# Optimization experiments

Hardware: AMD Instinct MI355X
Metric: run time of the kernel (lower is better)

## Reference

```python
import math
import jax, jax.numpy as jnp
import numpy as np

B, S, D, N, H = 4, 1024, 1024, 16, 64

def setup_inputs() -> dict:
    key = jax.random.key(0)
    ks = jax.random.split(key, 10)
    sc = 0.02
    return {
        'from_tensor': jax.random.normal(ks[0], (B, S, D), jnp.float32),
        'to_tensor': jax.random.normal(ks[1], (B, S, D), jnp.float32),
        'attention_mask': jnp.ones((B, S, S), jnp.int32),
        'wq': jax.random.normal(ks[2], (D, N, H), jnp.float32) * sc,
        'bq': jnp.zeros((N, H), jnp.float32),
        'wk': jax.random.normal(ks[3], (D, N, H), jnp.float32) * sc,
        'bk': jnp.zeros((N, H), jnp.float32),
        'wv': jax.random.normal(ks[4], (D, N, H), jnp.float32) * sc,
        'bv': jnp.zeros((N, H), jnp.float32),
        'pre_softmax_weight': jax.random.normal(ks[5], (N, N), jnp.float32) * sc,
        'post_softmax_weight': jax.random.normal(ks[6], (N, N), jnp.float32) * sc,
        'wo': jax.random.normal(ks[7], (N, H, D), jnp.float32) * sc,
        'bo': jnp.zeros((D,), jnp.float32),
    }

def reference(from_tensor, to_tensor, attention_mask, wq, bq, wk, bk, wv, bv,
              pre_softmax_weight, post_softmax_weight, wo, bo):
    # QKV projections: [B,S,D] x [D,N,H] -> [B,S,N,H]
    q = jnp.einsum('bfd,dnh->bfnh', from_tensor, wq) + bq
    k = jnp.einsum('btd,dnh->btnh', to_tensor, wk) + bk
    v = jnp.einsum('btd,dnh->btnh', to_tensor, wv) + bv
    # attention scores [B,N,F,T]
    scores = jnp.einsum('btnh,bfnh->bnft', k, q) * (1.0 / math.sqrt(float(H)))
    # pre-softmax head mixing
    scores = jnp.einsum('bnft,nl->blft', scores, pre_softmax_weight)
    # masked softmax (mask expanded at axis 1, additive -10000 on masked)
    mask = attention_mask.astype(scores.dtype)[:, None, :, :]  # [B,1,F,T]
    scores = scores + (1.0 - mask) * -10000.0
    probs = jax.nn.softmax(scores, axis=-1)
    # post-softmax head mixing (dropout rate 0.0 -> identity)
    probs = jnp.einsum('bnft,nl->blft', probs, post_softmax_weight)
    # attend to values and project out
    ctx = jnp.einsum('bnft,btnh->bfnh', probs, v)
    out = jnp.einsum('bfnh,nhd->bfd', ctx, wo) + bo
    return out
```

## Files before the change

kernel.cpp:

```cpp
#include <hip/hip_runtime.h>
#include <hip/hip_bf16.h>

typedef __hip_bfloat16 bf16;
using short8 = __attribute__((ext_vector_type(8))) short;
using f32x4  = __attribute__((ext_vector_type(4))) float;
using f32x2  = __attribute__((ext_vector_type(2))) float;

#ifndef __has_builtin
#define __has_builtin(x) 0
#endif
#if __has_builtin(__builtin_amdgcn_global_load_lds)
#define HAVE_GLL 1
#else
#define HAVE_GLL 0
#endif

__device__ inline void stage16(const short* __restrict__ g, short* l, int lane) {
#if HAVE_GLL
  __builtin_amdgcn_global_load_lds((__attribute__((address_space(1))) void*)g,
                                   (__attribute__((address_space(3))) void*)l,
                                   16, 0, 0);
#else
  *(short8*)(l + lane * 8) = *(const short8*)g;
#endif
}

__device__ inline unsigned pack2bf(float a, float b) {
  bf16 h0 = __float2bfloat16(a), h1 = __float2bfloat16(b);
  return (unsigned)*(unsigned short*)&h0 | ((unsigned)*(unsigned short*)&h1 << 16);
}

__global__ __launch_bounds__(256) void gemm_lds64(
    const bf16* __restrict__ Ag, long a_bs1, long a_bs2, int lda,
    const bf16* __restrict__ Bg, long b_bs1, long b_bs2, int ldb,
    void* __restrict__ Cg, long c_bs1, long c_bs2, int ldc,
    const float* __restrict__ bias, int K, int Z2, float alpha, int cf32)
{
  __shared__ short As[128 * 64];
  __shared__ short Bs[64 * 64];

  int z = blockIdx.z, z1 = z / Z2, z2 = z - z1 * Z2;
  const short* A = (const short*)(Ag + z1 * a_bs1 + z2 * a_bs2);
  const short* B = (const short*)(Bg + z1 * b_bs1 + z2 * b_bs2);

  int tid = threadIdx.x, lane = tid & 63, w = tid >> 6;
  int wm = w & 1, wn = w >> 1;
  int m0 = blockIdx.x * 128, n0 = blockIdx.y * 64;
  int r = lane & 15, q = lane >> 4;

  int srow = lane >> 3, scol = (lane & 7) * 8;
  const short* Asrc = A + (long)(m0 + w * 32 + srow) * lda + scol;
  const short* Bsrc = B + (long)(n0 + w * 16 + srow) * ldb + scol;
  short* Adst = As + (w * 32) * 64;
  short* Bdst = Bs + (w * 16) * 64;

  f32x4 acc[4][2];
  #pragma unroll
  for (int i = 0; i < 4; ++i)
    #pragma unroll
    for (int j = 0; j < 2; ++j) acc[i][j] = (f32x4){0.f, 0.f, 0.f, 0.f};

  for (int kt = 0; kt < K; kt += 64) {
    #pragma unroll
    for (int i = 0; i < 4; ++i)
      stage16(Asrc + (long)i * 8 * lda + kt, Adst + i * 8 * 64, lane);
    #pragma unroll
    for (int i = 0; i < 2; ++i)
      stage16(Bsrc + (long)i * 8 * ldb + kt, Bdst + i * 8 * 64, lane);
    __syncthreads();
    #pragma unroll
    for (int kk = 0; kk < 64; kk += 32) {
      short8 af[4], bfr[2];
      #pragma unroll
      for (int i = 0; i < 4; ++i)
        af[i] = *(const short8*)&As[(wm * 64 + i * 16 + r) * 64 + kk + q * 8];
      #pragma unroll
      for (int j = 0; j < 2; ++j)
        bfr[j] = *(const short8*)&Bs[(wn * 32 + j * 16 + r) * 64 + kk + q * 8];
      #pragma unroll
      for (int i = 0; i < 4; ++i)
        #pragma unroll
        for (int j = 0; j < 2; ++j)
          acc[i][j] = __builtin_amdgcn_mfma_f32_16x16x32_bf16(af[i], bfr[j], acc[i][j], 0, 0, 0);
    }
    __syncthreads();
  }

  long cb = z1 * c_bs1 + z2 * c_bs2;
  #pragma unroll
  for (int j = 0; j < 2; ++j) {
    int col = n0 + wn * 32 + j * 16 + r;
    float bv = bias ? bias[col] : 0.0f;
    #pragma unroll
    for (int i = 0; i < 4; ++i) {
      int row0 = m0 + wm * 64 + i * 16 + q * 4;
      #pragma unroll
      for (int rr = 0; rr < 4; ++rr) {
        float val = acc[i][j][rr] * alpha + bv;
        long idx = cb + (long)(row0 + rr) * ldc + col;
        if (cf32) ((float*)Cg)[idx] = val;
        else ((bf16*)Cg)[idx] = __float2bfloat16(val);
      }
    }
  }
}

struct QKVArgs {
  const bf16* A[3];
  const bf16* Bw[3];
  bf16* C[3];
  const float* bias[3];
};

__global__ __launch_bounds__(256) void gemm_qkv(QKVArgs args) {
  __shared__ short As[128 * 64];
  __shared__ short Bs[64 * 64];

  int z = blockIdx.z;
  const short* A = (const short*)args.A[z];
  const short* B = (const short*)args.Bw[z];
  bf16* C = args.C[z];
  const float* bias = args.bias[z];

  int tid = threadIdx.x, lane = tid & 63, w = tid >> 6;
  int wm = w & 1, wn = w >> 1;
  int m0 = blockIdx.x * 128, n0 = blockIdx.y * 64;
  int r = lane & 15, q = lane >> 4;

  int srow = lane >> 3, scol = (lane & 7) * 8;
  const short* Asrc = A + (long)(m0 + w * 32 + srow) * 1024 + scol;
  const short* Bsrc = B + (long)(n0 + w * 16 + srow) * 1024 + scol;
  short* Adst = As + (w * 32) * 64;
  short* Bdst = Bs + (w * 16) * 64;

  f32x4 acc[4][2];
  #pragma unroll
  for (int i = 0; i < 4; ++i)
    #pragma unroll
    for (int j = 0; j < 2; ++j) acc[i][j] = (f32x4){0.f, 0.f, 0.f, 0.f};

  for (int kt = 0; kt < 1024; kt += 64) {
    #pragma unroll
    for (int i = 0; i < 4; ++i)
      stage16(Asrc + (long)i * 8 * 1024 + kt, Adst + i * 8 * 64, lane);
    #pragma unroll
    for (int i = 0; i < 2; ++i)
      stage16(Bsrc + (long)i * 8 * 1024 + kt, Bdst + i * 8 * 64, lane);
    __syncthreads();
    #pragma unroll
    for (int kk = 0; kk < 64; kk += 32) {
      short8 af[4], bfr[2];
      #pragma unroll
      for (int i = 0; i < 4; ++i)
        af[i] = *(const short8*)&As[(wm * 64 + i * 16 + r) * 64 + kk + q * 8];
      #pragma unroll
      for (int j = 0; j < 2; ++j)
        bfr[j] = *(const short8*)&Bs[(wn * 32 + j * 16 + r) * 64 + kk + q * 8];
      #pragma unroll
      for (int i = 0; i < 4; ++i)
        #pragma unroll
        for (int j = 0; j < 2; ++j)
          acc[i][j] = __builtin_amdgcn_mfma_f32_16x16x32_bf16(af[i], bfr[j], acc[i][j], 0, 0, 0);
    }
    __syncthreads();
  }

  #pragma unroll
  for (int j = 0; j < 2; ++j) {
    int col = n0 + wn * 32 + j * 16 + r;
    float bv = bias[col];
    #pragma unroll
    for (int i = 0; i < 4; ++i) {
      int row0 = m0 + wm * 64 + i * 16 + q * 4;
      #pragma unroll
      for (int rr = 0; rr < 4; ++rr)
        C[(long)(row0 + rr) * 1024 + col] = __float2bfloat16(acc[i][j][rr] + bv);
    }
  }
}

__global__ __launch_bounds__(256) void gemm_k64(
    const bf16* __restrict__ Ag, long a_bs1, long a_bs2, int lda,
    const bf16* __restrict__ Bg, long b_bs1, long b_bs2, int ldb,
    bf16* __restrict__ Cg, long c_bs1, long c_bs2, int ldc,
    int Z2, float alpha)
{
  int z = blockIdx.z, z1 = z / Z2, z2 = z - z1 * Z2;
  const short* A = (const short*)(Ag + z1 * a_bs1 + z2 * a_bs2);
  const short* B = (const short*)(Bg + z1 * b_bs1 + z2 * b_bs2);
  bf16* C = Cg + z1 * c_bs1 + z2 * c_bs2;

  int tid = threadIdx.x, lane = tid & 63, w = tid >> 6;
  int wm = w & 1, wn = w >> 1;
  int m0 = blockIdx.x * 128 + wm * 64;
  int n0 = blockIdx.y * 128 + wn * 64;
  int r = lane & 15, q = lane >> 4;

  const short* Ar = A + (long)(m0 + r) * lda + q * 8;
  const short* Br = B + (long)(n0 + r) * ldb + q * 8;

  f32x4 acc[4][4];
  #pragma unroll
  for (int i = 0; i < 4; ++i)
    #pragma unroll
    for (int j = 0; j < 4; ++j) acc[i][j] = (f32x4){0.f, 0.f, 0.f, 0.f};

  #pragma unroll
  for (int kk = 0; kk < 64; kk += 32) {
    short8 af[4], bfr[4];
    #pragma unroll
    for (int i = 0; i < 4; ++i) af[i] = *(const short8*)(Ar + (long)i * 16 * lda + kk);
    #pragma unroll
    for (int j = 0; j < 4; ++j) bfr[j] = *(const short8*)(Br + (long)j * 16 * ldb + kk);
    #pragma unroll
    for (int i = 0; i < 4; ++i)
      #pragma unroll
      for (int j = 0; j < 4; ++j)
        acc[i][j] = __builtin_amdgcn_mfma_f32_16x16x32_bf16(af[i], bfr[j], acc[i][j], 0, 0, 0);
  }

  #pragma unroll
  for (int j = 0; j < 4; ++j) {
    int col = n0 + j * 16 + r;
    #pragma unroll
    for (int i = 0; i < 4; ++i) {
      int row0 = m0 + i * 16 + q * 4;
      #pragma unroll
      for (int rr = 0; rr < 4; ++rr)
        C[(long)(row0 + rr) * ldc + col] = __float2bfloat16(acc[i][j][rr] * alpha);
    }
  }
}

__global__ __launch_bounds__(256) void cvt2(
    const float* __restrict__ a, const float* __restrict__ b,
    bf16* __restrict__ oa, bf16* __restrict__ ob)
{
  const float* in = blockIdx.y ? b : a;
  bf16* out = blockIdx.y ? ob : oa;
  int i = (blockIdx.x * 256 + threadIdx.x) * 8;
  float4 v0 = *(const float4*)(in + i);
  float4 v1 = *(const float4*)(in + i + 4);
  uint4 pk;
  pk.x = pack2bf(v0.x, v0.y);
  pk.y = pack2bf(v0.z, v0.w);
  pk.z = pack2bf(v1.x, v1.y);
  pk.w = pack2bf(v1.z, v1.w);
  *(uint4*)(out + i) = pk;
}

struct WT4 { const float* s[4]; bf16* d[4]; };

__global__ __launch_bounds__(256) void wtrans4(WT4 a) {
  __shared__ bf16 tile[64][66];
  int z = blockIdx.z;
  const float* in = a.s[z];
  bf16* out = a.d[z];
  int r0 = blockIdx.x * 64, c0 = blockIdx.y * 64;
  int tx = threadIdx.x & 63, ty = threadIdx.x >> 6;
  #pragma unroll
  for (int i = 0; i < 16; ++i) {
    int rr = i * 4 + ty;
    tile[rr][tx] = __float2bfloat16(in[(long)(r0 + rr) * 1024 + c0 + tx]);
  }
  __syncthreads();
  #pragma unroll
  for (int i = 0; i < 16; ++i) {
    int rr = i * 4 + ty;
    out[(long)(c0 + rr) * 1024 + r0 + tx] = tile[tx][rr];
  }
}

__global__ __launch_bounds__(256) void transpose_bf16(
    const bf16* __restrict__ in, long i_bs1, long i_bs2, int i_rs,
    bf16* __restrict__ out, long o_bs1, long o_bs2, int o_rs, int Z2)
{
  __shared__ bf16 tile[64][66];
  int z = blockIdx.z, z1 = z / Z2, z2 = z - z1 * Z2;
  const bf16* ib = in + z1 * i_bs1 + z2 * i_bs2;
  bf16* ob = out + z1 * o_bs1 + z2 * o_bs2;
  int r0 = blockIdx.x * 64, c0 = blockIdx.y * 64;
  int tx = threadIdx.x & 63, ty = threadIdx.x >> 6;
  #pragma unroll
  for (int i = 0; i < 16; ++i) {
    int rr = i * 4 + ty;
    tile[rr][tx] = ib[(long)(r0 + rr) * i_rs + c0 + tx];
  }
  __syncthreads();
  #pragma unroll
  for (int i = 0; i < 16; ++i) {
    int rr = i * 4 + ty;
    ob[(long)(c0 + rr) * o_rs + r0 + tx] = tile[tx][rr];
  }
}

__global__ __launch_bounds__(512) void mixsoftmax6(
    bf16* __restrict__ sc, long sc_bs, const float* __restrict__ pre,
    const float* __restrict__ post, const int* __restrict__ mask)
{
  __shared__ short Sb[1024][24];
  __shared__ float wpreS[256], wpostS[256];
  __shared__ float zred[8][16];
  __shared__ float zinvs[16];

  int tid = threadIdx.x;
  int lane = tid & 63, w = tid >> 6;
  int g = lane >> 4;
  int l = lane & 15;
  int f = blockIdx.x, b = blockIdx.y;

  unsigned short* scb = (unsigned short*)(sc + (long)b * sc_bs) + ((long)f << 10);
  const int* mk = mask + ((long)b << 20) + ((long)f << 10);
  int tg = tid * 2;

  if (tid < 256) {
    wpreS[tid] = pre[tid];
    wpostS[tid] = post[tid];
  }

  #pragma unroll
  for (int n = 0; n < 16; ++n) {
    int nn = (n + (tid & 12)) & 15;
    unsigned uu = *(const unsigned*)(scb + ((long)nn << 20) + tg);
    Sb[tg][nn]     = (short)(uu & 0xffffu);
    Sb[tg + 1][nn] = (short)(uu >> 16);
  }
  __syncthreads();

  short8 af1;
  #pragma unroll
  for (int i = 0; i < 8; ++i) {
    int n = ((g & 1) << 3) + i;
    bf16 hv = __float2bfloat16(wpreS[n * 16 + l]);
    af1[i] = (g < 2) ? *(short*)&hv : (short)0;
  }

  f32x4 zacc = (f32x4){0.f, 0.f, 0.f, 0.f};
  int tb = w * 128 + l;
  #pragma unroll
  for (int it = 0; it < 8; ++it) {
    int t0 = tb + it * 16;
    short8 bfr = *(const short8*)&Sb[t0][(g & 1) * 8];
    float madd = (1.0f - (float)mk[t0]) * -10000.0f;
    f32x4 cin = (f32x4){madd, madd, madd, madd};
    f32x4 a = __builtin_amdgcn_mfma_f32_16x16x32_bf16(af1, bfr, cin, 0, 0, 0);
    f32x4 e;
    #pragma unroll
    for (int j = 0; j < 4; ++j) e[j] = __expf(a[j]);
    zacc += e;
    uint2 pk;
    pk.x = pack2bf(e[0], e[1]);
    pk.y = pack2bf(e[2], e[3]);
    *(uint2*)&Sb[t0][g * 4] = pk;
  }

  #pragma unroll
  for (int m = 1; m < 16; m <<= 1) {
    #pragma unroll
    for (int j = 0; j < 4; ++j) zacc[j] += __shfl_xor(zacc[j], m, 64);
  }
  if (l == 0) *(f32x4*)&zred[w][g * 4] = zacc;
  __syncthreads();
  if (tid < 16) {
    float z = 0.f;
    #pragma unroll
    for (int ww = 0; ww < 8; ++ww) z += zred[ww][tid];
    zinvs[tid] = 1.0f / z;
  }
  __syncthreads();

  short8 af2;
  #pragma unroll
  for (int i = 0; i < 8; ++i) {
    int n = ((g & 1) << 3) + i;
    bf16 hv = __float2bfloat16(wpostS[n * 16 + l] * zinvs[n]);
    af2[i] = (g < 2) ? *(short*)&hv : (short)0;
  }

  #pragma unroll
  for (int it = 0; it < 8; ++it) {
    int t0 = tb + it * 16;
    short8 bE = *(const short8*)&Sb[t0][(g & 1) * 8];
    f32x4 o = __builtin_amdgcn_mfma_f32_16x16x32_bf16(
        af2, bE, (f32x4){0.f, 0.f, 0.f, 0.f}, 0, 0, 0);
    #pragma unroll
    for (int j = 0; j < 4; ++j) {
      bf16 hv = __float2bfloat16(o[j]);
      scb[((long)(g * 4 + j) << 20) + t0] = *(unsigned short*)&hv;
    }
  }
}

extern "C" void kernel_launch(void* const* d_in, const int* in_sizes, int n_in,
                              void* d_out, int out_size, void* d_ws, size_t ws_size,
                              hipStream_t stream) {
  const float* from = (const float*)d_in[0];
  const float* to   = (const float*)d_in[1];
  const int*  mask  = (const int*)d_in[2];
  const float* wq = (const float*)d_in[3];
  const float* bq = (const float*)d_in[4];
  const float* wk = (const float*)d_in[5];
  const float* bk = (const float*)d_in[6];
  const float* wv = (const float*)d_in[7];
  const float* bv = (const float*)d_in[8];
  const float* pre  = (const float*)d_in[9];
  const float* post = (const float*)d_in[10];
  const float* wo = (const float*)d_in[11];
  const float* bo = (const float*)d_in[12];
  float* out = (float*)d_out;

  bf16* W = (bf16*)d_ws;
  const long M1 = 1048576;
  bool big = ws_size >= (size_t)(85 * M1) * 2;

  bf16 *Sc, *fromB, *toB, *wqT, *wkT, *wvT, *woT, *Q, *Kp, *V, *Vt, *ctx;
  if (big) {
    Sc = W;                 fromB = W;            toB = W + 4 * M1;
    wqT = W + 8 * M1;       wkT = W + 9 * M1;     wvT = W + 10 * M1;
    woT = W + 64 * M1;      Q = W + 65 * M1;      Kp = W + 69 * M1;
    V = W + 73 * M1;        Vt = W + 77 * M1;     ctx = W + 81 * M1;
  } else {
    Sc = W;                 fromB = W;            toB = W + 4 * M1;
    wqT = W + 8 * M1;       wkT = W + 9 * M1;     wvT = W + 10 * M1;
    woT = W + 16 * M1;      Q = W + 17 * M1;      Kp = W + 21 * M1;
    V = W + 25 * M1;        Vt = W + 29 * M1;     ctx = W + 33 * M1;
  }

  dim3 blk(256);

  cvt2<<<dim3(2048, 2), blk, 0, stream>>>(from, to, fromB, toB);
  WT4 wt;
  wt.s[0] = wq; wt.s[1] = wk; wt.s[2] = wv; wt.s[3] = wo;
  wt.d[0] = wqT; wt.d[1] = wkT; wt.d[2] = wvT; wt.d[3] = woT;
  wtrans4<<<dim3(16, 16, 4), blk, 0, stream>>>(wt);

  QKVArgs qa;
  qa.A[0] = fromB; qa.A[1] = toB; qa.A[2] = toB;
  qa.Bw[0] = wqT;  qa.Bw[1] = wkT; qa.Bw[2] = wvT;
  qa.C[0] = Q;     qa.C[1] = Kp;  qa.C[2] = V;
  qa.bias[0] = bq; qa.bias[1] = bk; qa.bias[2] = bv;
  gemm_qkv<<<dim3(32, 16, 3), blk, 0, stream>>>(qa);

  transpose_bf16<<<dim3(16, 1, 64), blk, 0, stream>>>(V, M1, 64, 1024,
                                                      Vt, M1, 65536, 1024, 16);

  if (big) {
    gemm_k64<<<dim3(8, 8, 64), blk, 0, stream>>>(
        Q, M1, 64, 1024, Kp, M1, 64, 1024, Sc, 16 * M1, M1, 1024, 16, 0.125f);
    mixsoftmax6<<<dim3(1024, 4), dim3(512), 0, stream>>>(Sc, 16 * M1, pre, post, mask);
    gemm_lds64<<<dim3(8, 1, 64), blk, 0, stream>>>(
        Sc, 16 * M1, M1, 1024, Vt, M1, 65536, 1024, ctx, M1, 64, 1024, nullptr,
        1024, 16, 1.0f, 0);
  } else {
    for (int b = 0; b < 4; ++b) {
      gemm_k64<<<dim3(8, 8, 16), blk, 0, stream>>>(
          Q + b * M1, 0, 64, 1024, Kp + b * M1, 0, 64, 1024,
          Sc, 0, M1, 1024, 16, 0.125f);
      mixsoftmax6<<<dim3(1024, 1), dim3(512), 0, stream>>>(Sc, 0, pre, post, mask + b * M1);
      gemm_lds64<<<dim3(8, 1, 16), blk, 0, stream>>>(
          Sc, 0, M1, 1024, Vt + b * M1, 0, 65536, 1024,
          ctx + b * M1, 0, 64, 1024, nullptr, 1024, 16, 1.0f, 0);
    }
  }

  gemm_lds64<<<dim3(32, 16, 1), blk, 0, stream>>>(
      ctx, 0, 0, 1024, woT, 0, 0, 1024, out, 0, 0, 1024, bo, 1024, 1, 1.0f, 1);
}
```

Baseline: 343.3 us.

## Restructure mix-softmax kernel into two pipelined chunks with smaller LDS footprint

Result: faster. 331.8 us (-3.3%).

```diff
diff --git a/kernel.cpp b/kernel.cpp
--- a/kernel.cpp
+++ b/kernel.cpp
@@ -294,72 +294,151 @@
   }
 }
 
-__global__ __launch_bounds__(512) void mixsoftmax6(
+__device__ inline void wrows7(short* rowE, short* rowO, const unsigned* ld) {
+  union { unsigned u[4]; short8 s; } cv;
+  cv.u[0] = (ld[0] & 0xffffu) | (ld[1] << 16);
+  cv.u[1] = (ld[2] & 0xffffu) | (ld[3] << 16);
+  cv.u[2] = (ld[4] & 0xffffu) | (ld[5] << 16);
+  cv.u[3] = (ld[6] & 0xffffu) | (ld[7] << 16);
+  *(short8*)rowE = cv.s;
+  uint2 d0, d1;
+  d0.x = (ld[0] >> 16) | (ld[1] & 0xffff0000u);
+  d0.y = (ld[2] >> 16) | (ld[3] & 0xffff0000u);
+  d1.x = (ld[4] >> 16) | (ld[5] & 0xffff0000u);
+  d1.y = (ld[6] >> 16) | (ld[7] & 0xffff0000u);
+  *(uint2*)rowO = d0;
+  *(uint2*)(rowO + 4) = d1;
+}
+
+template<int C>
+__device__ inline void compute_chunk7(const short* Sb, const int* mk, int tb,
+    int g, short8 af1, f32x4& zacc, unsigned (&epk)[8][2]) {
+  #pragma unroll
+  for (int it = 0; it < 4; ++it) {
+    int tl = tb + it * 16;
+    const short* rp = Sb + tl * 20 + (g & 1) * 8;
+    union { uint2 u2[2]; short8 s; } cv;
+    cv.u2[0] = *(const uint2*)rp;
+    cv.u2[1] = *(const uint2*)(rp + 4);
+    float m = (float)mk[C * 512 + tl];
+    float madd = (1.0f - m) * -14426.9504f;
+    f32x4 a = __builtin_amdgcn_mfma_f32_16x16x32_bf16(
+        af1, cv.s, (f32x4){madd, madd, madd, madd}, 0, 0, 0);
+    f32x4 e;
+    #pragma unroll
+    for (int j = 0; j < 4; ++j) e[j] = exp2f(a[j]);
+    zacc += e;
+    epk[C * 4 + it][0] = pack2bf(e[0], e[1]);
+    epk[C * 4 + it][1] = pack2bf(e[2], e[3]);
+  }
+}
+
+template<int C>
+__device__ inline void pass2_chunk7(short* Sb, unsigned short* scb, int tb,
+    int g, short8 af2, const unsigned (&epk)[8][2],
+    const short* rowE, const short* rowO, int nh, int p) {
+  #pragma unroll
+  for (int it = 0; it < 4; ++it) {
+    int tl = tb + it * 16;
+    uint2 ev; ev.x = epk[C * 4 + it][0]; ev.y = epk[C * 4 + it][1];
+    *(uint2*)(Sb + tl * 20 + g * 4) = ev;
+  }
+  asm volatile("s_waitcnt lgkmcnt(0)" ::: "memory");
+  __builtin_amdgcn_sched_barrier(0);
+  #pragma unroll
+  for (int it = 0; it < 4; ++it) {
+    int tl = tb + it * 16;
+    const short* rp = Sb + tl * 20 + (g & 1) * 8;
+    union { uint2 u2[2]; short8 s; } cv;
+    cv.u2[0] = *(const uint2*)rp;
+    cv.u2[1] = *(const uint2*)(rp + 4);
+    f32x4 o = __builtin_amdgcn_mfma_f32_16x16x32_bf16(
+        af2, cv.s, (f32x4){0.f, 0.f, 0.f, 0.f}, 0, 0, 0);
+    uint2 dv; dv.x = pack2bf(o[0], o[1]); dv.y = pack2bf(o[2], o[3]);
+    *(uint2*)(Sb + tl * 20 + g * 4) = dv;
+  }
+  __syncthreads();
+  union { uint2 u2[2]; unsigned u[4]; short8 s; } de;
+  de.s = *(const short8*)rowE;
+  uint2 q0 = *(const uint2*)rowO;
+  uint2 q1 = *(const uint2*)(rowO + 4);
+  unsigned od[4] = {q0.x, q0.y, q1.x, q1.y};
+  #pragma unroll
+  for (int jj = 0; jj < 4; ++jj) {
+    unsigned evw = de.u[jj], odw = od[jj];
+    unsigned out0 = (evw & 0xffffu) | (odw << 16);
+    unsigned out1 = (evw >> 16) | (odw & 0xffff0000u);
+    int n0 = nh * 8 + jj * 2;
+    *(unsigned*)(scb + ((long)n0 << 20) + C * 512 + 2 * p) = out0;
+    *(unsigned*)(scb + ((long)(n0 + 1) << 20) + C * 512 + 2 * p) = out1;
+  }
+}
+
+__global__ __launch_bounds__(512, 8) void mixsoftmax7(
     bf16* __restrict__ sc, long sc_bs, const float* __restrict__ pre,
     const float* __restrict__ post, const int* __restrict__ mask)
 {
-  __shared__ short Sb[1024][24];
+  __shared__ short Sb[512 * 20];
   __shared__ float wpreS[256], wpostS[256];
   __shared__ float zred[8][16];
   __shared__ float zinvs[16];
 
   int tid = threadIdx.x;
   int lane = tid & 63, w = tid >> 6;
-  int g = lane >> 4;
-  int l = lane & 15;
+  int g = lane >> 4, r = lane & 15;
   int f = blockIdx.x, b = blockIdx.y;
 
   unsigned short* scb = (unsigned short*)(sc + (long)b * sc_bs) + ((long)f << 10);
   const int* mk = mask + ((long)b << 20) + ((long)f << 10);
-  int tg = tid * 2;
 
   if (tid < 256) {
-    wpreS[tid] = pre[tid];
+    wpreS[tid] = pre[tid] * 1.44269504f;
     wpostS[tid] = post[tid];
   }
 
-  #pragma unroll
-  for (int n = 0; n < 16; ++n) {
-    int nn = (n + (tid & 12)) & 15;
-    unsigned uu = *(const unsigned*)(scb + ((long)nn << 20) + tg);
-    Sb[tg][nn]     = (short)(uu & 0xffffu);
-    Sb[tg + 1][nn] = (short)(uu >> 16);
-  }
+  int nh = tid >> 8, p = tid & 255;
+  const unsigned short* sAddr = scb + ((long)(nh * 8) << 20) + 2 * p;
+  short* rowE = &Sb[(2 * p) * 20 + nh * 8];
+  short* rowO = &Sb[(2 * p + 1) * 20 + nh * 8];
+
+  int tb = w * 64 + r;
+
+  unsigned epk[8][2];
+  f32x4 zacc = (f32x4){0.f, 0.f, 0.f, 0.f};
+
+  unsigned ld[8];
+  #pragma unroll
+  for (int i = 0; i < 8; ++i)
+    ld[i] = *(const unsigned*)(sAddr + ((long)i << 20));
   __syncthreads();
 
   short8 af1;
   #pragma unroll
   for (int i = 0; i < 8; ++i) {
     int n = ((g & 1) << 3) + i;
-    bf16 hv = __float2bfloat16(wpreS[n * 16 + l]);
+    bf16 hv = __float2bfloat16(wpreS[n * 16 + r]);
     af1[i] = (g < 2) ? *(short*)&hv : (short)0;
   }
 
-  f32x4 zacc = (f32x4){0.f, 0.f, 0.f, 0.f};
-  int tb = w * 128 + l;
-  #pragma unroll
-  for (int it = 0; it < 8; ++it) {
-    int t0 = tb + it * 16;
-    short8 bfr = *(const short8*)&Sb[t0][(g & 1) * 8];
-    float madd = (1.0f - (float)mk[t0]) * -10000.0f;
-    f32x4 cin = (f32x4){madd, madd, madd, madd};
-    f32x4 a = __builtin_amdgcn_mfma_f32_16x16x32_bf16(af1, bfr, cin, 0, 0, 0);
-    f32x4 e;
-    #pragma unroll
-    for (int j = 0; j < 4; ++j) e[j] = __expf(a[j]);
-    zacc += e;
-    uint2 pk;
-    pk.x = pack2bf(e[0], e[1]);
-    pk.y = pack2bf(e[2], e[3]);
-    *(uint2*)&Sb[t0][g * 4] = pk;
-  }
-
-  #pragma unroll
-  for (int m = 1; m < 16; m <<= 1) {
-    #pragma unroll
-    for (int j = 0; j < 4; ++j) zacc[j] += __shfl_xor(zacc[j], m, 64);
-  }
-  if (l == 0) *(f32x4*)&zred[w][g * 4] = zacc;
+  wrows7(rowE, rowO, ld);
+  __syncthreads();
+
+  #pragma unroll
+  for (int i = 0; i < 8; ++i)
+    ld[i] = *(const unsigned*)(sAddr + ((long)i << 20) + 512);
+
+  compute_chunk7<0>(Sb, mk, tb, g, af1, zacc, epk);
+  __syncthreads();
+  wrows7(rowE, rowO, ld);
+  __syncthreads();
+  compute_chunk7<1>(Sb, mk, tb, g, af1, zacc, epk);
+
+  #pragma unroll
+  for (int m2 = 1; m2 < 16; m2 <<= 1) {
+    #pragma unroll
+    for (int j = 0; j < 4; ++j) zacc[j] += __shfl_xor(zacc[j], m2, 64);
+  }
+  if (r == 0) *(f32x4*)&zred[w][g * 4] = zacc;
   __syncthreads();
   if (tid < 16) {
     float z = 0.f;
@@ -373,22 +452,13 @@
   #pragma unroll
   for (int i = 0; i < 8; ++i) {
     int n = ((g & 1) << 3) + i;
-    bf16 hv = __float2bfloat16(wpostS[n * 16 + l] * zinvs[n]);
+    bf16 hv = __float2bfloat16(wpostS[n * 16 + r] * zinvs[n]);
     af2[i] = (g < 2) ? *(short*)&hv : (short)0;
   }
 
-  #pragma unroll
-  for (int it = 0; it < 8; ++it) {
-    int t0 = tb + it * 16;
-    short8 bE = *(const short8*)&Sb[t0][(g & 1) * 8];
-    f32x4 o = __builtin_amdgcn_mfma_f32_16x16x32_bf16(
-        af2, bE, (f32x4){0.f, 0.f, 0.f, 0.f}, 0, 0, 0);
-    #pragma unroll
-    for (int j = 0; j < 4; ++j) {
-      bf16 hv = __float2bfloat16(o[j]);
-      scb[((long)(g * 4 + j) << 20) + t0] = *(unsigned short*)&hv;
-    }
-  }
+  pass2_chunk7<0>(Sb, scb, tb, g, af2, epk, rowE, rowO, nh, p);
+  __syncthreads();
+  pass2_chunk7<1>(Sb, scb, tb, g, af2, epk, rowE, rowO, nh, p);
 }
 
 extern "C" void kernel_launch(void* const* d_in, const int* in_sizes, int n_in,
@@ -447,7 +517,7 @@
   if (big) {
     gemm_k64<<<dim3(8, 8, 64), blk, 0, stream>>>(
         Q, M1, 64, 1024, Kp, M1, 64, 1024, Sc, 16 * M1, M1, 1024, 16, 0.125f);
-    mixsoftmax6<<<dim3(1024, 4), dim3(512), 0, stream>>>(Sc, 16 * M1, pre, post, mask);
+    mixsoftmax7<<<dim3(1024, 4), dim3(512), 0, stream>>>(Sc, 16 * M1, pre, post, mask);
     gemm_lds64<<<dim3(8, 1, 64), blk, 0, stream>>>(
         Sc, 16 * M1, M1, 1024, Vt, M1, 65536, 1024, ctx, M1, 64, 1024, nullptr,
         1024, 16, 1.0f, 0);
@@ -456,7 +526,7 @@
       gemm_k64<<<dim3(8, 8, 16), blk, 0, stream>>>(
           Q + b * M1, 0, 64, 1024, Kp + b * M1, 0, 64, 1024,
           Sc, 0, M1, 1024, 16, 0.125f);
-      mixsoftmax6<<<dim3(1024, 1), dim3(512), 0, stream>>>(Sc, 0, pre, post, mask + b * M1);
+      mixsoftmax7<<<dim3(1024, 1), dim3(512), 0, stream>>>(Sc, 0, pre, post, mask + b * M1);
       gemm_lds64<<<dim3(8, 1, 16), blk, 0, stream>>>(
           Sc, 0, M1, 1024, Vt + b * M1, 0, 65536, 1024,
           ctx + b * M1, 0, 64, 1024, nullptr, 1024, 16, 1.0f, 0);
```
